# Performance work log

Measured on AMD Instinct MI355X. Metric: run time of the kernel, lower is better.

Reference implementation:

```python
import jax, jax.numpy as jnp
import numpy as np

H, W = 85, 85
N_HEAD = 8

def layernorm(x, g, b, eps=1e-5):
    m = x.mean(-1, keepdims=True)
    v = ((x - m) ** 2).mean(-1, keepdims=True)
    return (x - m) * jax.lax.rsqrt(v + eps) * g + b


def setup_inputs() -> dict:
    key = jax.random.key(0)
    ks = jax.random.split(key, 12)
    B, C = 8, 256
    N = H * W
    hd = C // N_HEAD
    Ch = C * 4  # mlp_ratio = 4
    init = lambda k, fan_in, sh: (jax.random.normal(k, sh, jnp.float32) / np.float32(np.sqrt(fan_in)))
    d = {}
    d['fx'] = jax.random.normal(ks[0], (B, N, C), jnp.float32)
    # ln_1
    d['ln1_g'] = jnp.ones((C,), jnp.float32); d['ln1_b'] = jnp.zeros((C,), jnp.float32)
    # Galerkin linear attention projections (per-head split of C)
    d['Wq'] = init(ks[1], C, (C, C)); d['bq'] = jnp.zeros((C,), jnp.float32)
    d['Wk'] = init(ks[2], C, (C, C)); d['bk'] = jnp.zeros((C,), jnp.float32)
    d['Wv'] = init(ks[3], C, (C, C)); d['bv'] = jnp.zeros((C,), jnp.float32)
    d['Wo'] = init(ks[4], C, (C, C)); d['bo'] = jnp.zeros((C,), jnp.float32)
    # per-head LayerNorms on K and V (Galerkin normalization replacing softmax)
    d['kln_g'] = jnp.ones((N_HEAD, hd), jnp.float32); d['kln_b'] = jnp.zeros((N_HEAD, hd), jnp.float32)
    d['vln_g'] = jnp.ones((N_HEAD, hd), jnp.float32); d['vln_b'] = jnp.zeros((N_HEAD, hd), jnp.float32)
    # ln_2
    d['ln2_g'] = jnp.ones((C,), jnp.float32); d['ln2_b'] = jnp.zeros((C,), jnp.float32)
    # MLP (n_layers=0, res=False): pre linear + gelu, post linear
    d['W1'] = init(ks[5], C, (C, Ch)); d['b1'] = jnp.zeros((Ch,), jnp.float32)
    d['W2'] = init(ks[6], Ch, (Ch, C)); d['b2'] = jnp.zeros((C,), jnp.float32)
    return d


def reference(fx, ln1_g, ln1_b, Wq, bq, Wk, bk, Wv, bv, Wo, bo,
              kln_g, kln_b, vln_g, vln_b, ln2_g, ln2_b, W1, b1, W2, b2):
    B, N, C = fx.shape
    hd = C // N_HEAD
    x = layernorm(fx, ln1_g, ln1_b)  # [B,N,C]
    # (permute/reshape to image grid and back is a no-op for per-token attention math)
    split = lambda t: t.reshape(B, N, N_HEAD, hd).transpose(0, 2, 1, 3)  # [B,h,N,d]
    q = split(x @ Wq + bq)
    k = split(x @ Wk + bk)
    v = split(x @ Wv + bv)
    # Galerkin: LayerNorm on K and V over head dim, no softmax
    k = layernorm(k, kln_g[None, :, None, :], kln_b[None, :, None, :])
    v = layernorm(v, vln_g[None, :, None, :], vln_b[None, :, None, :])
    kv = jnp.einsum('bhnd,bhne->bhde', k, v) / N  # [B,h,d,d]
    attn = jnp.einsum('bhnd,bhde->bhne', q, kv)   # [B,h,N,d]
    attn = attn.transpose(0, 2, 1, 3).reshape(B, N, C)
    attn = attn @ Wo + bo
    fx = fx + attn  # residual 1
    x2 = layernorm(fx, ln2_g, ln2_b)
    x2 = jax.nn.gelu(x2 @ W1 + b1) @ W2 + b2
    return fx + x2  # residual 2
```

## Files before the change

### kernel.cpp

```cpp
#include <hip/hip_runtime.h>
#include <hip/hip_bf16.h>
#include <stdint.h>

#define B_ 8
#define NTOK 7225
#define MTOT (B_*NTOK)
#define MROWS 58368
#define MT_FULL 226
#define MT_BATCH 29
#define MLP_TILES 904

typedef unsigned short u16;
typedef u16 u16x8 __attribute__((ext_vector_type(8)));
typedef u16 u16x4 __attribute__((ext_vector_type(4)));
typedef __bf16 bf16x8 __attribute__((ext_vector_type(8)));
typedef float f32x4 __attribute__((ext_vector_type(4)));

__device__ inline float bf2f(u16 u){ union{float f;uint32_t i;}c; c.i=((uint32_t)u)<<16; return c.f; }
__device__ inline u16 f2bf(float f){ union{float f;uint32_t i;}c; c.f=f; uint32_t x=c.i;
                                     return (u16)((x + 0x7fffu + ((x>>16)&1u))>>16); }
__device__ inline uint32_t cvt_pk_bf16(float a, float b){
  uint32_t r; asm("v_cvt_pk_bf16_f32 %0, %1, %2" : "=v"(r) : "v"(a), "v"(b)); return r;
}
__device__ inline float gelu_f(float x){
  float t = 0.7978845608028654f * x * (1.0f + 0.044715f*x*x);
  float e = __expf(2.0f*t);
  return x * (1.0f - __builtin_amdgcn_rcpf(e + 1.0f));
}

__device__ inline void gload_lds16(const u16* g, u16* l) {
  __builtin_amdgcn_global_load_lds(
      (__attribute__((address_space(1))) void*)(const_cast<u16*>(g)),
      (__attribute__((address_space(3))) void*)(l), 16, 0, 0);
}

template<int EPI>
__global__ __launch_bounds__(512, 2)
void gemm256(const u16* __restrict__ A, int lda,
             const u16* __restrict__ Bm, int ldb, long bStride,
             const float* __restrict__ bias, int biasStride,
             const float* __restrict__ res,
             void* __restrict__ outp, int ldo,
             int K, int rowsValid, int batchRowStride,
             const float* __restrict__ g2, const float* __restrict__ b2,
             u16* __restrict__ x2out)
{
  __shared__ alignas(16) u16 lds[65536];
  const int tid = threadIdx.x;
  const int wid = tid >> 6, lane = tid & 63;
  const int wm = wid >> 2, wn = wid & 3;

  const int gx = gridDim.x, gy = gridDim.y;
  const int n = gx * gy;
  const int flat = blockIdx.y * gx + blockIdx.x;
  const int qq = n >> 3, rr = n & 7;
  const int xcd = flat & 7, pos = flat >> 3;
  const int swz = (xcd < rr ? xcd*(qq+1) : rr*(qq+1) + (xcd-rr)*qq) + pos;
  const int bx = swz / gy, by = swz % gy;
  const int bz = blockIdx.z;

  const long rowBase = (long)bz * batchRowStride + (long)bx * 256;
  const int colBase = by * 256;
  const u16* Bp = Bm + (long)bz * bStride;
  const float* biasP = bias + bz * biasStride;

  const int srow = lane >> 2;
  const int scol = ((lane & 3) ^ ((lane >> 3) & 3)) * 8;
  const int NT = K >> 6;

  auto stageHalf = [&](int bf, int kt, int sel) {
    const int sub = sel >> 1;
    const int k0 = (kt << 6) + sub*32 + scol;
    u16* base = lds + ((sel & 1) ? 32768 : 0) + (bf*2 + sub)*8192;
#pragma unroll
    for (int i = 0; i < 2; ++i) {
      const int r0 = (wid*2 + i)*16;
      if ((sel & 1) == 0)
        gload_lds16(A + (rowBase + r0 + srow)*(long)lda + k0, base + r0*32);
      else
        gload_lds16(Bp + (long)(colBase + r0 + srow)*ldb + k0, base + r0*32);
    }
  };

  f32x4 acc[8][4] = {};
  bf16x8 afr[4], bfr[4];
  const int lr = lane & 15;
  const int sl = lane >> 4;
  const int sp = (sl ^ ((lr >> 1) & 3)) * 8;

  stageHalf(0, 0, 0); stageHalf(0, 0, 1); stageHalf(0, 0, 2); stageHalf(0, 0, 3);

  for (int kt = 0; kt < NT; ++kt) {
    const int bf = kt & 1;
    const bool st = (kt + 1 < NT);
#pragma unroll
    for (int ph = 0; ph < 4; ++ph) {
      const int sub = ph >> 1, mh = ph & 1;
      if (ph == 0) {
        asm volatile("s_waitcnt vmcnt(4)" ::: "memory");
      } else if (ph == 2) {
        if (kt == NT - 1) asm volatile("s_waitcnt vmcnt(0)" ::: "memory");
        else              asm volatile("s_waitcnt vmcnt(4)" ::: "memory");
      } else {
        asm volatile("s_waitcnt vmcnt(6)" ::: "memory");
      }
      __builtin_amdgcn_s_barrier();
      const u16* Ab = lds + (bf*2 + sub)*8192;
      const u16* Bb = lds + 32768 + (bf*2 + sub)*8192;
      if (mh == 0) {
#pragma unroll
        for (int ni = 0; ni < 4; ++ni)
          bfr[ni] = *reinterpret_cast<const bf16x8*>(&Bb[(wn*64 + ni*16 + lr)*32 + sp]);
      }
#pragma unroll
      for (int i = 0; i < 4; ++i)
        afr[i] = *reinterpret_cast<const bf16x8*>(&Ab[(wm*128 + (mh*4 + i)*16 + lr)*32 + sp]);
      if (st) stageHalf(bf ^ 1, kt + 1, ph);
      asm volatile("s_waitcnt lgkmcnt(0)" ::: "memory");
      __builtin_amdgcn_sched_barrier(0);
      __builtin_amdgcn_s_setprio(1);
#pragma unroll
      for (int i = 0; i < 4; ++i)
#pragma unroll
        for (int ni = 0; ni < 4; ++ni)
          acc[mh*4 + i][ni] =
              __builtin_amdgcn_mfma_f32_16x16x32_bf16(bfr[ni], afr[i], acc[mh*4 + i][ni], 0, 0, 0);
      __builtin_amdgcn_s_setprio(0);
    }
  }

  const int cq = sl * 4;
  if (EPI <= 1) {
    __syncthreads();
#pragma unroll
    for (int mi = 0; mi < 8; ++mi) {
      const int r = wm*128 + mi*16 + lr;
#pragma unroll
      for (int ni = 0; ni < 4; ++ni) {
        const int c = wn*64 + ni*16 + cq;
        f32x4 v = acc[mi][ni] + *reinterpret_cast<const f32x4*>(&biasP[colBase + c]);
        uint2 pk;
        if (EPI == 1) { pk.x = cvt_pk_bf16(gelu_f(v[0]), gelu_f(v[1]));
                        pk.y = cvt_pk_bf16(gelu_f(v[2]), gelu_f(v[3])); }
        else          { pk.x = cvt_pk_bf16(v[0], v[1]); pk.y = cvt_pk_bf16(v[2], v[3]); }
        const int unit = ((c >> 3) ^ (r & 7));
        *reinterpret_cast<uint2*>(lds + r*256 + unit*8 + (c & 7)) = pk;
      }
    }
    __syncthreads();
#pragma unroll
    for (int p = 0; p < 16; ++p) {
      const int idx = p*512 + tid;
      const int r = idx >> 5, u = idx & 31;
      const int phys = u ^ (r & 7);
      u16x8 val = *reinterpret_cast<const u16x8*>(lds + r*256 + phys*8);
      *reinterpret_cast<u16x8*>((u16*)outp + (rowBase + r)*(long)ldo + colBase + u*8) = val;
    }
  } else {
    float* red = reinterpret_cast<float*>(lds);
    __syncthreads();
#pragma unroll
    for (int mi = 0; mi < 8; ++mi) {
      const int r = wm*128 + mi*16 + lr;
      const bool valid = (bx*256 + r < rowsValid);
      const long grow = rowBase + r;
      float s_r = 0.f, q_r = 0.f;
#pragma unroll
      for (int ni = 0; ni < 4; ++ni) {
        const int c0 = wn*64 + ni*16 + cq;
        f32x4 rv = valid ? *reinterpret_cast<const f32x4*>((const float*)res + grow*256 + c0)
                         : f32x4{0.f,0.f,0.f,0.f};
        f32x4 v = acc[mi][ni] + *reinterpret_cast<const f32x4*>(&biasP[c0]) + rv;
        acc[mi][ni] = v;
        s_r += v[0]+v[1]+v[2]+v[3];
        q_r += v[0]*v[0]+v[1]*v[1]+v[2]*v[2]+v[3]*v[3];
      }
      s_r += __shfl_xor(s_r, 16); s_r += __shfl_xor(s_r, 32);
      q_r += __shfl_xor(q_r, 16); q_r += __shfl_xor(q_r, 32);
      if (sl == 0) {
        red[       (wm*4 + wn)*128 + mi*16 + lr] = s_r;
        red[1024 + (wm*4 + wn)*128 + mi*16 + lr] = q_r;
      }
    }
    __syncthreads();
#pragma unroll
    for (int mi = 0; mi < 8; ++mi) {
      const int r = wm*128 + mi*16 + lr;
      if (bx*256 + r >= rowsValid) continue;
      const long grow = rowBase + r;
      const int rb = wm*4*128 + mi*16 + lr;
      float s_t = red[rb] + red[rb+128] + red[rb+256] + red[rb+384];
      float q_t = red[1024+rb] + red[1024+rb+128] + red[1024+rb+256] + red[1024+rb+384];
      const float m = s_t * (1.0f/256.0f);
      const float var = q_t * (1.0f/256.0f) - m*m;
      const float rs = rsqrtf(var + 1e-5f);
#pragma unroll
      for (int ni = 0; ni < 4; ++ni) {
        const int c0 = wn*64 + ni*16 + cq;
        const long oidx = grow*256 + c0;
        f32x4 v = acc[mi][ni];
        *reinterpret_cast<f32x4*>((float*)outp + oidx) = v;
        f32x4 gv = *reinterpret_cast<const f32x4*>(&g2[c0]);
        f32x4 bv = *reinterpret_cast<const f32x4*>(&b2[c0]);
        f32x4 xn = (v - m) * rs * gv + bv;
        uint2 pk; pk.x = cvt_pk_bf16(xn[0], xn[1]); pk.y = cvt_pk_bf16(xn[2], xn[3]);
        *reinterpret_cast<uint2*>(x2out + oidx) = pk;
      }
    }
  }
}

__global__ __launch_bounds__(512, 1)
void mlp_fused2(const u16* __restrict__ x2, const u16* __restrict__ W1t,
                const u16* __restrict__ W2t, const float* __restrict__ b1,
                const float* __restrict__ b2, float* __restrict__ outF,
                int rowsValid)
{
  __shared__ alignas(16) u16 Xs[64*256];
  __shared__ alignas(16) u16 Wsb[32768];
  __shared__ alignas(16) u16 Hs[64*128];
  const int tid = threadIdx.x;
  const int wid = tid >> 6, lane = tid & 63;
  const int wm = wid >> 1, wn = wid & 1;
  const int lr = lane & 15, sl = lane >> 4;
  const long rowBase = (long)blockIdx.x * 64;
  const int rA = wm*16 + lr;

#pragma unroll
  for (int i = 0; i < 4; ++i) {
    const int u = i*512 + tid;
    const int r = u >> 5, pu = u & 31;
    gload_lds16(x2 + (rowBase + r)*256 + ((pu ^ (r & 31)) << 3), &Xs[u*8]);
  }
  auto stageW1 = [&](int c) {
#pragma unroll
    for (int i = 0; i < 8; ++i) {
      const int u = i*512 + tid;
      const int r = u >> 5, pu = u & 31;
      gload_lds16(W1t + (long)(c*128 + r)*256 + ((pu ^ (r & 31)) << 3), &Wsb[u*8]);
    }
  };
  auto stageW2 = [&](int c) {
#pragma unroll
    for (int i = 0; i < 8; ++i) {
      const int u = i*512 + tid;
      const int r = u >> 4, pu = u & 15;
      gload_lds16(W2t + (long)r*1024 + c*128 + ((pu ^ (r & 15)) << 3), &Wsb[u*8]);
    }
  };
  stageW1(0);
  asm volatile("s_waitcnt vmcnt(0)" ::: "memory");
  __syncthreads();

  f32x4 acc2[8] = {};
  for (int c = 0; c < 8; ++c) {
    f32x4 acc1[4] = {};
#pragma unroll
    for (int kk = 0; kk < 8; ++kk) {
      const int u = kk*4 + sl;
      bf16x8 xa = *reinterpret_cast<const bf16x8*>(&Xs[(rA*32 + (u ^ (rA & 31)))*8]);
#pragma unroll
      for (int ni = 0; ni < 4; ++ni) {
        const int rB = wn*64 + ni*16 + lr;
        bf16x8 wb = *reinterpret_cast<const bf16x8*>(&Wsb[(rB*32 + (u ^ (rB & 31)))*8]);
        acc1[ni] = __builtin_amdgcn_mfma_f32_16x16x32_bf16(wb, xa, acc1[ni], 0, 0, 0);
      }
    }
    __builtin_amdgcn_s_barrier();
    stageW2(c);
    const float* b1c = b1 + c*128;
#pragma unroll
    for (int ni = 0; ni < 4; ++ni) {
      const int col = wn*64 + ni*16 + sl*4;
      f32x4 v = acc1[ni] + *reinterpret_cast<const f32x4*>(&b1c[col]);
      uint2 pk; pk.x = cvt_pk_bf16(gelu_f(v[0]), gelu_f(v[1]));
      pk.y = cvt_pk_bf16(gelu_f(v[2]), gelu_f(v[3]));
      const int uw = (col >> 3) ^ (rA & 15);
      *reinterpret_cast<uint2*>(&Hs[rA*128 + uw*8 + (col & 7)]) = pk;
    }
    asm volatile("s_waitcnt vmcnt(0)" ::: "memory");
    __syncthreads();
#pragma unroll
    for (int kk = 0; kk < 4; ++kk) {
      const int u = kk*4 + sl;
      bf16x8 ha = *reinterpret_cast<const bf16x8*>(&Hs[(rA*16 + (u ^ (rA & 15)))*8]);
#pragma unroll
      for (int nj = 0; nj < 8; ++nj) {
        const int rB = wn*128 + nj*16 + lr;
        bf16x8 wb = *reinterpret_cast<const bf16x8*>(&Wsb[(rB*16 + (u ^ (rB & 15)))*8]);
        acc2[nj] = __builtin_amdgcn_mfma_f32_16x16x32_bf16(wb, ha, acc2[nj], 0, 0, 0);
      }
    }
    __builtin_amdgcn_s_barrier();
    if (c + 1 < 8) {
      stageW1(c + 1);
      asm volatile("s_waitcnt vmcnt(0)" ::: "memory");
      __syncthreads();
    }
  }
  if (rowBase + rA < rowsValid) {
    float* orow = outF + (rowBase + rA)*256;
#pragma unroll
    for (int nj = 0; nj < 8; ++nj) {
      const int col = wn*128 + nj*16 + sl*4;
      f32x4 v = acc2[nj] + *reinterpret_cast<const f32x4*>(&b2[col])
              + *reinterpret_cast<const f32x4*>(&orow[col]);
      *reinterpret_cast<f32x4*>(&orow[col]) = v;
    }
  }
}

__global__ __launch_bounds__(256)
void ln_kernel(const float* __restrict__ in, const float* __restrict__ g,
               const float* __restrict__ bt, u16* __restrict__ out, int M)
{
  const int wv = threadIdx.x >> 6, lane = threadIdx.x & 63;
  const int t = blockIdx.x * 4 + wv;
  if (t >= M) return;
  const float4 x = reinterpret_cast<const float4*>(in + (long)t*256)[lane];
  float s = x.x + x.y + x.z + x.w;
  float q = x.x*x.x + x.y*x.y + x.z*x.z + x.w*x.w;
#pragma unroll
  for (int o = 32; o > 0; o >>= 1) { s += __shfl_xor(s, o); q += __shfl_xor(q, o); }
  const float m  = s * (1.0f/256.0f);
  const float var = q * (1.0f/256.0f) - m*m;
  const float rs = rsqrtf(var + 1e-5f);
  const float4 gv = reinterpret_cast<const float4*>(g)[lane];
  const float4 bv = reinterpret_cast<const float4*>(bt)[lane];
  uint2 o4;
  o4.x = cvt_pk_bf16((x.x - m)*rs*gv.x + bv.x, (x.y - m)*rs*gv.y + bv.y);
  o4.y = cvt_pk_bf16((x.z - m)*rs*gv.z + bv.z, (x.w - m)*rs*gv.w + bv.w);
  *reinterpret_cast<uint2*>(out + (long)t*256 + lane*4) = o4;
}

__global__ __launch_bounds__(256)
void kv_kernel(const u16* __restrict__ KV,
               const float* __restrict__ kg, const float* __restrict__ kb,
               const float* __restrict__ vg, const float* __restrict__ vb,
               float* __restrict__ kvout)
{
  const int bh = blockIdx.x, b = bh >> 3, h = bh & 7;
  const int tid = threadIdx.x;
  __shared__ u16 kls[256][32];
  __shared__ u16 vls[256][32];
  __shared__ float sg[4][32];
  if (tid < 32) {
    sg[0][tid] = kg[h*32 + tid];
    sg[1][tid] = kb[h*32 + tid];
    sg[2][tid] = vg[h*32 + tid];
    sg[3][tid] = vb[h*32 + tid];
  }
  const int d = tid >> 3, e0 = (tid & 7) * 4;
  float a0=0, a1=0, a2=0, a3=0;

  for (int sub = 0; sub < 2; ++sub) {
    const int r = blockIdx.y * 512 + sub * 256 + tid;
    __syncthreads();
    if (r < NTOK) {
      const u16* rowp = KV + (long)(b*NTOK + r)*512;
#pragma unroll
      for (int kv2 = 0; kv2 < 2; ++kv2) {
        const u16* p = rowp + (kv2 ? 256 : 0) + h*32;
        float xv[32]; float s = 0.f;
#pragma unroll
        for (int q4 = 0; q4 < 4; ++q4) {
          u16x8 u = *reinterpret_cast<const u16x8*>(p + q4*8);
#pragma unroll
          for (int j = 0; j < 8; ++j) { float f = bf2f(u[j]); xv[q4*8+j] = f; s += f; }
        }
        const float m = s * (1.0f/32.0f);
        float vv = 0.f;
#pragma unroll
        for (int j = 0; j < 32; ++j) { float d2 = xv[j]-m; vv += d2*d2; }
        const float rs = rsqrtf(vv*(1.0f/32.0f) + 1e-5f);
        const float* gg = sg[kv2 ? 2 : 0];
        const float* bb = sg[kv2 ? 3 : 1];
        u16 (*dst)[32] = kv2 ? vls : kls;
#pragma unroll
        for (int j = 0; j < 32; ++j) dst[tid][j] = f2bf((xv[j]-m)*rs*gg[j] + bb[j]);
      }
    } else {
#pragma unroll
      for (int j = 0; j < 32; ++j) { kls[tid][j] = 0; vls[tid][j] = 0; }
    }
    __syncthreads();
#pragma unroll 4
    for (int rr = 0; rr < 256; ++rr) {
      const float kd = bf2f(kls[rr][d]);
      u16x4 v4 = *reinterpret_cast<const u16x4*>(&vls[rr][e0]);
      a0 += kd * bf2f(v4[0]); a1 += kd * bf2f(v4[1]);
      a2 += kd * bf2f(v4[2]); a3 += kd * bf2f(v4[3]);
    }
  }
  const float sc = 1.0f / (float)NTOK;
  float* o = kvout + (long)bh*1024 + d*32 + e0;
  atomicAdd(o+0, a0*sc); atomicAdd(o+1, a1*sc);
  atomicAdd(o+2, a2*sc); atomicAdd(o+3, a3*sc);
}

__global__ __launch_bounds__(256)
void woeff_kernel(const float* __restrict__ kv, const float* __restrict__ Wo,
                  u16* __restrict__ Woet)
{
  const int b = blockIdx.x >> 8, c = blockIdx.x & 255;
  const int rtid = threadIdx.x;
  const int h = rtid >> 5, dd = rtid & 31;
  const float* kvp = kv + ((long)(b*8 + h)*32 + dd)*32;
  float s = 0.f;
#pragma unroll 8
  for (int e = 0; e < 32; ++e) s += kvp[e] * Wo[(h*32 + e)*256 + c];
  Woet[(long)(b*256 + c)*256 + rtid] = f2bf(s);
}

__global__ __launch_bounds__(256)
void watt_kernel(const u16* __restrict__ wq_bf, const u16* __restrict__ Woet,
                 u16* __restrict__ Watt)
{
  const int b = blockIdx.x >> 8, c = blockIdx.x & 255;
  const int k = threadIdx.x;
  const u16* wr = wq_bf + (long)k*256;
  const u16* er = Woet + ((long)(b*256 + c))*256;
  float s = 0.f;
#pragma unroll 4
  for (int j0 = 0; j0 < 256; j0 += 8) {
    u16x8 wv = *reinterpret_cast<const u16x8*>(wr + j0);
    u16x8 ev = *reinterpret_cast<const u16x8*>(er + j0);
#pragma unroll
    for (int j = 0; j < 8; ++j) s += bf2f(wv[j]) * bf2f(ev[j]);
  }
  Watt[((long)(b*256 + c))*256 + k] = f2bf(s);
}

__global__ __launch_bounds__(256)
void be_kernel(const float* __restrict__ bq, const float* __restrict__ bo,
               const u16* __restrict__ Woet, float* __restrict__ be)
{
  const int b = blockIdx.x, c = threadIdx.x;
  const u16* er = Woet + ((long)(b*256 + c))*256;
  float s = bo[c];
#pragma unroll 4
  for (int j0 = 0; j0 < 256; j0 += 8) {
    u16x8 ev = *reinterpret_cast<const u16x8*>(er + j0);
#pragma unroll
    for (int j = 0; j < 8; ++j) s += bq[j0+j] * bf2f(ev[j]);
  }
  be[b*256 + c] = s;
}

__device__ void transpose_tile(const float* __restrict__ src, u16* __restrict__ dst,
                               int R, int C, int tcx, int trY)
{
  __shared__ float t[32][33];
  const int tc = tcx * 32, tr = trY * 32;
  const int lx = threadIdx.x & 31, ly = threadIdx.x >> 5;
#pragma unroll
  for (int i = 0; i < 32; i += 8)
    t[ly + i][lx] = src[(long)(tr + ly + i)*C + tc + lx];
  __syncthreads();
#pragma unroll
  for (int i = 0; i < 32; i += 8)
    dst[(long)(tc + ly + i)*R + tr + lx] = f2bf(t[lx][ly + i]);
}

__global__ __launch_bounds__(256)
void prep_kernel(const float* __restrict__ Wk, const float* __restrict__ Wv,
                 const float* __restrict__ W1, const float* __restrict__ W2,
                 const float* __restrict__ Wq,
                 const float* __restrict__ bk, const float* __restrict__ bv,
                 u16* __restrict__ Wkv_t, u16* __restrict__ W1_t, u16* __restrict__ W2_t,
                 u16* __restrict__ wq_bf, float* __restrict__ kvb, float* __restrict__ bkv)
{
  int b = blockIdx.x;
  if (b < 256)      { transpose_tile(W1, W1_t, 256, 1024, b & 31, b >> 5); }
  else if (b < 512) { b -= 256; transpose_tile(W2, W2_t, 1024, 256, b & 7, b >> 3); }
  else if (b < 576) { b -= 512; transpose_tile(Wk, Wkv_t,         256, 256, b & 7, b >> 3); }
  else if (b < 640) { b -= 576; transpose_tile(Wv, Wkv_t + 65536, 256, 256, b & 7, b >> 3); }
  else if (b < 648) {
    const int base = (b - 640) * 8192 + threadIdx.x;
#pragma unroll
    for (int i = 0; i < 32; ++i) wq_bf[base + i*256] = f2bf(Wq[base + i*256]);
  } else if (b < 656) {
    const int base = (b - 648) * 8192 + threadIdx.x;
#pragma unroll
    for (int i = 0; i < 32; ++i) kvb[base + i*256] = 0.f;
  } else {
    const int i = threadIdx.x;
    bkv[i] = bk[i]; bkv[256 + i] = bv[i];
  }
}

extern "C" void kernel_launch(void* const* d_in, const int* in_sizes, int n_in,
                              void* d_out, int out_size, void* d_ws, size_t ws_size,
                              hipStream_t stream)
{
  const float* fx    = (const float*)d_in[0];
  const float* ln1_g = (const float*)d_in[1];
  const float* ln1_b = (const float*)d_in[2];
  const float* Wq = (const float*)d_in[3];
  const float* bq = (const float*)d_in[4];
  const float* Wk = (const float*)d_in[5];
  const float* bk = (const float*)d_in[6];
  const float* Wv = (const float*)d_in[7];
  const float* bv = (const float*)d_in[8];
  const float* Wo = (const float*)d_in[9];
  const float* bo = (const float*)d_in[10];
  const float* kg  = (const float*)d_in[11];
  const float* kbb = (const float*)d_in[12];
  const float* vg  = (const float*)d_in[13];
  const float* vbb = (const float*)d_in[14];
  const float* ln2_g = (const float*)d_in[15];
  const float* ln2_b = (const float*)d_in[16];
  const float* W1 = (const float*)d_in[17];
  const float* b1 = (const float*)d_in[18];
  const float* W2 = (const float*)d_in[19];
  const float* b2 = (const float*)d_in[20];
  float* outF = (float*)d_out;

  char* ws = (char*)d_ws;
  size_t off = 0;
  auto alloc = [&](size_t bytes) { char* p = ws + off; off += (bytes + 255) & ~(size_t)255; return p; };
  u16* bufX   = (u16*)alloc((size_t)MROWS*256*2);
  u16* bufKV  = (u16*)alloc((size_t)MROWS*512*2);
  u16* Wkv_t  = (u16*)alloc(512*256*2);
  u16* W1_t   = (u16*)alloc(1024*256*2);
  u16* W2_t   = (u16*)alloc(256*1024*2);
  u16* Woe_t  = (u16*)alloc((size_t)8*256*256*2);
  u16* Watt   = (u16*)alloc((size_t)8*256*256*2);
  u16* wq_bf  = (u16*)alloc(256*256*2);
  float* kvb  = (float*)alloc((size_t)64*1024*4);
  float* bkv  = (float*)alloc(512*4);
  float* be   = (float*)alloc(8*256*4);
  (void)ws_size; (void)out_size; (void)n_in; (void)in_sizes;

  prep_kernel<<<657, 256, 0, stream>>>(Wk, Wv, W1, W2, Wq, bk, bv,
                                       Wkv_t, W1_t, W2_t, wq_bf, kvb, bkv);

  ln_kernel<<<MTOT/4, 256, 0, stream>>>(fx, ln1_g, ln1_b, bufX, MTOT);

  gemm256<0><<<dim3(MT_FULL, 2, 1), 512, 0, stream>>>(
      bufX, 256, Wkv_t, 256, 0, bkv, 0, nullptr, bufKV, 512, 256, MTOT, 0,
      nullptr, nullptr, nullptr);

  kv_kernel<<<dim3(64, 15), 256, 0, stream>>>(bufKV, kg, kbb, vg, vbb, kvb);

  woeff_kernel<<<2048, 256, 0, stream>>>(kvb, Wo, Woe_t);
  watt_kernel<<<2048, 256, 0, stream>>>(wq_bf, Woe_t, Watt);
  be_kernel<<<8, 256, 0, stream>>>(bq, bo, Woe_t, be);

  gemm256<3><<<dim3(MT_BATCH, 1, 8), 512, 0, stream>>>(
      bufX, 256, Watt, 256, 65536, be, 256, fx, outF, 256, 256, NTOK, NTOK,
      ln2_g, ln2_b, bufX);

  mlp_fused2<<<MLP_TILES, 512, 0, stream>>>(bufX, W1_t, W2_t, b1, b2, outF, MTOT);
}
```

Baseline: 318.0 us.

## Double-buffer W1 chunks and split W2 buffer in fused MLP kernel

Restructures the fused MLP kernel to walk the hidden dimension in 16 chunks of 64 instead of 8 chunks of 128. W1 gets a double buffer and W2 its own buffer, so the next W1 chunk and the current W2 chunk load asynchronously while compute runs, using partial vmcnt waits in place of full drains. The warp tiling changes to 2x4, with each wave covering two 16-row M tiles to get register reuse of the weight fragments. This adds more barriers per chunk and depends on the exact vmcnt counts being right.

```diff
diff --git a/kernel.cpp b/kernel.cpp
--- a/kernel.cpp
+++ b/kernel.cpp
@@ -211,20 +211,20 @@
 }
 
 __global__ __launch_bounds__(512, 1)
-void mlp_fused2(const u16* __restrict__ x2, const u16* __restrict__ W1t,
+void mlp_fused3(const u16* __restrict__ x2, const u16* __restrict__ W1t,
                 const u16* __restrict__ W2t, const float* __restrict__ b1,
                 const float* __restrict__ b2, float* __restrict__ outF,
                 int rowsValid)
 {
   __shared__ alignas(16) u16 Xs[64*256];
-  __shared__ alignas(16) u16 Wsb[32768];
-  __shared__ alignas(16) u16 Hs[64*128];
+  __shared__ alignas(16) u16 W1b[2][64*256];
+  __shared__ alignas(16) u16 W2b[256*64];
+  __shared__ alignas(16) u16 Hs[64*64];
   const int tid = threadIdx.x;
   const int wid = tid >> 6, lane = tid & 63;
-  const int wm = wid >> 1, wn = wid & 1;
+  const int wm = wid >> 2, wn = wid & 3;
   const int lr = lane & 15, sl = lane >> 4;
   const long rowBase = (long)blockIdx.x * 64;
-  const int rA = wm*16 + lr;
 
 #pragma unroll
   for (int i = 0; i < 4; ++i) {
@@ -232,80 +232,94 @@
     const int r = u >> 5, pu = u & 31;
     gload_lds16(x2 + (rowBase + r)*256 + ((pu ^ (r & 31)) << 3), &Xs[u*8]);
   }
-  auto stageW1 = [&](int c) {
-#pragma unroll
-    for (int i = 0; i < 8; ++i) {
+  auto stageW1 = [&](int c, int half) {
+#pragma unroll
+    for (int i = 0; i < 4; ++i) {
       const int u = i*512 + tid;
       const int r = u >> 5, pu = u & 31;
-      gload_lds16(W1t + (long)(c*128 + r)*256 + ((pu ^ (r & 31)) << 3), &Wsb[u*8]);
+      gload_lds16(W1t + (long)(c*64 + r)*256 + ((pu ^ (r & 31)) << 3), &W1b[half][u*8]);
     }
   };
   auto stageW2 = [&](int c) {
 #pragma unroll
-    for (int i = 0; i < 8; ++i) {
+    for (int i = 0; i < 4; ++i) {
       const int u = i*512 + tid;
-      const int r = u >> 4, pu = u & 15;
-      gload_lds16(W2t + (long)r*1024 + c*128 + ((pu ^ (r & 15)) << 3), &Wsb[u*8]);
+      const int r = u >> 3, pu = u & 7;
+      gload_lds16(W2t + (long)r*1024 + c*64 + ((pu ^ (r & 7)) << 3), &W2b[u*8]);
     }
   };
-  stageW1(0);
-  asm volatile("s_waitcnt vmcnt(0)" ::: "memory");
-  __syncthreads();
-
-  f32x4 acc2[8] = {};
-  for (int c = 0; c < 8; ++c) {
-    f32x4 acc1[4] = {};
+  stageW1(0, 0);
+
+  f32x4 acc2[2][4] = {};
+  for (int c = 0; c < 16; ++c) {
+    const int half = c & 1;
+    const bool st = (c + 1 < 16);
+    stageW2(c);
+    if (st) stageW1(c + 1, half ^ 1);
+    if (st) asm volatile("s_waitcnt vmcnt(8)" ::: "memory");
+    else    asm volatile("s_waitcnt vmcnt(4)" ::: "memory");
+    __builtin_amdgcn_s_barrier();
+
+    f32x4 acc1[2] = {};
 #pragma unroll
     for (int kk = 0; kk < 8; ++kk) {
       const int u = kk*4 + sl;
-      bf16x8 xa = *reinterpret_cast<const bf16x8*>(&Xs[(rA*32 + (u ^ (rA & 31)))*8]);
-#pragma unroll
-      for (int ni = 0; ni < 4; ++ni) {
-        const int rB = wn*64 + ni*16 + lr;
-        bf16x8 wb = *reinterpret_cast<const bf16x8*>(&Wsb[(rB*32 + (u ^ (rB & 31)))*8]);
-        acc1[ni] = __builtin_amdgcn_mfma_f32_16x16x32_bf16(wb, xa, acc1[ni], 0, 0, 0);
-      }
-    }
-    __builtin_amdgcn_s_barrier();
-    stageW2(c);
-    const float* b1c = b1 + c*128;
-#pragma unroll
-    for (int ni = 0; ni < 4; ++ni) {
-      const int col = wn*64 + ni*16 + sl*4;
-      f32x4 v = acc1[ni] + *reinterpret_cast<const f32x4*>(&b1c[col]);
+      const int rB = wn*16 + lr;
+      bf16x8 wb = *reinterpret_cast<const bf16x8*>(&W1b[half][(rB*32 + (u ^ (rB & 31)))*8]);
+#pragma unroll
+      for (int mi = 0; mi < 2; ++mi) {
+        const int rA = wm*32 + mi*16 + lr;
+        bf16x8 xa = *reinterpret_cast<const bf16x8*>(&Xs[(rA*32 + (u ^ (rA & 31)))*8]);
+        acc1[mi] = __builtin_amdgcn_mfma_f32_16x16x32_bf16(wb, xa, acc1[mi], 0, 0, 0);
+      }
+    }
+    const float* b1c = b1 + c*64;
+#pragma unroll
+    for (int mi = 0; mi < 2; ++mi) {
+      const int r = wm*32 + mi*16 + lr;
+      const int col = wn*16 + sl*4;
+      f32x4 v = acc1[mi] + *reinterpret_cast<const f32x4*>(&b1c[col]);
       uint2 pk; pk.x = cvt_pk_bf16(gelu_f(v[0]), gelu_f(v[1]));
       pk.y = cvt_pk_bf16(gelu_f(v[2]), gelu_f(v[3]));
-      const int uw = (col >> 3) ^ (rA & 15);
-      *reinterpret_cast<uint2*>(&Hs[rA*128 + uw*8 + (col & 7)]) = pk;
-    }
-    asm volatile("s_waitcnt vmcnt(0)" ::: "memory");
-    __syncthreads();
-#pragma unroll
-    for (int kk = 0; kk < 4; ++kk) {
-      const int u = kk*4 + sl;
-      bf16x8 ha = *reinterpret_cast<const bf16x8*>(&Hs[(rA*16 + (u ^ (rA & 15)))*8]);
-#pragma unroll
-      for (int nj = 0; nj < 8; ++nj) {
-        const int rB = wn*128 + nj*16 + lr;
-        bf16x8 wb = *reinterpret_cast<const bf16x8*>(&Wsb[(rB*16 + (u ^ (rB & 15)))*8]);
-        acc2[nj] = __builtin_amdgcn_mfma_f32_16x16x32_bf16(wb, ha, acc2[nj], 0, 0, 0);
-      }
-    }
+      const int uw = (col >> 3) ^ (r & 7);
+      *reinterpret_cast<uint2*>(&Hs[r*64 + uw*8 + (col & 7)]) = pk;
+    }
+    if (st) asm volatile("s_waitcnt vmcnt(4) lgkmcnt(0)" ::: "memory");
+    else    asm volatile("s_waitcnt vmcnt(0) lgkmcnt(0)" ::: "memory");
     __builtin_amdgcn_s_barrier();
-    if (c + 1 < 8) {
-      stageW1(c + 1);
-      asm volatile("s_waitcnt vmcnt(0)" ::: "memory");
-      __syncthreads();
-    }
-  }
-  if (rowBase + rA < rowsValid) {
-    float* orow = outF + (rowBase + rA)*256;
-#pragma unroll
-    for (int nj = 0; nj < 8; ++nj) {
-      const int col = wn*128 + nj*16 + sl*4;
-      f32x4 v = acc2[nj] + *reinterpret_cast<const f32x4*>(&b2[col])
-              + *reinterpret_cast<const f32x4*>(&orow[col]);
-      *reinterpret_cast<f32x4*>(&orow[col]) = v;
+
+#pragma unroll
+    for (int kk2 = 0; kk2 < 2; ++kk2) {
+      const int u = kk2*4 + sl;
+      bf16x8 ha[2];
+#pragma unroll
+      for (int mi = 0; mi < 2; ++mi) {
+        const int r = wm*32 + mi*16 + lr;
+        ha[mi] = *reinterpret_cast<const bf16x8*>(&Hs[(r*8 + (u ^ (r & 7)))*8]);
+      }
+#pragma unroll
+      for (int nj = 0; nj < 4; ++nj) {
+        const int rB = wn*64 + nj*16 + lr;
+        bf16x8 wb = *reinterpret_cast<const bf16x8*>(&W2b[(rB*8 + (u ^ (rB & 7)))*8]);
+#pragma unroll
+        for (int mi = 0; mi < 2; ++mi)
+          acc2[mi][nj] = __builtin_amdgcn_mfma_f32_16x16x32_bf16(wb, ha[mi], acc2[mi][nj], 0, 0, 0);
+      }
+    }
+    __builtin_amdgcn_s_barrier();
+  }
+#pragma unroll
+  for (int mi = 0; mi < 2; ++mi) {
+    const int r = wm*32 + mi*16 + lr;
+    if (rowBase + r < rowsValid) {
+      float* orow = outF + (rowBase + r)*256;
+#pragma unroll
+      for (int nj = 0; nj < 4; ++nj) {
+        const int col = wn*64 + nj*16 + sl*4;
+        f32x4 v = acc2[mi][nj] + *reinterpret_cast<const f32x4*>(&b2[col])
+                + *reinterpret_cast<const f32x4*>(&orow[col]);
+        *reinterpret_cast<f32x4*>(&orow[col]) = v;
+      }
     }
   }
 }
@@ -551,5 +565,5 @@
       bufX, 256, Watt, 256, 65536, be, 256, fx, outF, 256, 256, NTOK, NTOK,
       ln2_g, ln2_b, bufX);
 
-  mlp_fused2<<<MLP_TILES, 512, 0, stream>>>(bufX, W1_t, W2_t, b1, b2, outF, MTOT);
-}
+  mlp_fused3<<<MLP_TILES, 512, 0, stream>>>(bufX, W1_t, W2_t, b1, b2, outF, MTOT);
+}
```

Measured after the change: 323.3 us. No clear change (+1.7%).
